# Optimization experiments

Measured on AMD Instinct MI355X. Metric: run time of the kernel, lower is better.

Reference implementation:

```python
import jax, jax.numpy as jnp
import numpy as np

B, N_CTX, NY, NX = 8, 1024, 128, 128
DIM_Y = 2
DOMAIN = 10.0


def setup_inputs() -> dict:
    key = jax.random.key(0)
    k1, k2 = jax.random.split(key)
    X_c = jax.random.uniform(k1, (B, N_CTX, 2), dtype=jnp.float32) * DOMAIN
    Y_c = jax.random.normal(k2, (B, N_CTX, DIM_Y), dtype=jnp.float32)
    ys = jnp.linspace(0.0, DOMAIN, NY, dtype=jnp.float32)
    xs = jnp.linspace(0.0, DOMAIN, NX, dtype=jnp.float32)
    gy, gx = jnp.meshgrid(ys, xs, indexing='ij')  # [NY,NX]
    grid = jnp.stack([gx, gy], axis=-1).reshape(-1, 2)  # [NY*NX, 2]
    log_l_scale = jnp.zeros((1,), dtype=jnp.float32)  # log(1.0)
    return {"X_c": X_c, "Y_c": Y_c, "grid": grid, "log_l_scale": log_l_scale}


def reference(X_c, Y_c, grid, log_l_scale):
    # l_scale = exp(clamp(log_l_scale, -5, 5))
    l = jnp.exp(jnp.clip(log_l_scale[0], -5.0, 5.0))
    # Pairwise squared distances grid-to-context: [B, G, N]
    diff = grid[None, :, None, :] - X_c[:, None, :, :]  # [B,G,N,2]
    d2 = jnp.sum(diff * diff, axis=-1)                  # [B,G,N]
    Gram = jnp.exp(-d2 / (2.0 * l * l))                 # RBF kernel
    # Expand Y with leading ones channel (density channel)
    ones = jnp.ones((B, N_CTX, 1), dtype=Y_c.dtype)
    Expand_Y = jnp.concatenate([ones, Y_c], axis=-1)    # [B,N,3]
    FM = jnp.einsum('bgn,bnc->bgc', Gram, Expand_Y)     # [B,G,3]
    density = FM[..., :1]
    feats = FM[..., 1:] / density                       # normalize by density
    FM = jnp.concatenate([density, feats], axis=-1)
    # reshape to image layout [B, C, NY, NX]
    return FM.reshape(B, NY, NX, DIM_Y + 1).transpose(0, 3, 1, 2)
```

## Files before the change

kernel.cpp:

```cpp
#include <hip/hip_runtime.h>


#define NCTX 1024
#define NG   128
#define NB   8
#define CH   64
#define STR  66

template<int NSPLIT>
__global__ __launch_bounds__(256, 2)
void eds_partial(const float* __restrict__ Xc,
                 const float* __restrict__ Yc,
                 const float* __restrict__ gridp,
                 const float* __restrict__ logl,
                 float* __restrict__ part)
{
    constexpr int SC = NCTX / NSPLIT;
    __shared__ float sEx[64 * STR];
    __shared__ float sEy[64 * STR];

    const int tid  = threadIdx.x;
    const int ixl  = tid & 15;
    const int iyl  = tid >> 4;
    const int lane = tid & 63;
    const int wv   = tid >> 6;

    int blk = blockIdx.x;
    const int s    = blk % NSPLIT;  blk /= NSPLIT;
    const int tile = blk & 3;
    const int b    = blk >> 2;
    const int tx0 = (tile & 1) * 64;
    const int ty0 = (tile >> 1) * 64;

    const float ls = fminf(5.0f, fmaxf(-5.0f, logl[0]));
    const float l  = expf(ls);
    const float scale = -0.7213475204444817f / (l * l);

    float d[16], a[16], c[16];
    #pragma unroll
    for (int i = 0; i < 16; ++i) { d[i] = 0.0f; a[i] = 0.0f; c[i] = 0.0f; }

    for (int ch = 0; ch < SC / CH; ++ch) {
        const int cb = s * SC + ch * CH;
        if (ch) __syncthreads();

        {
            const float gxr = gridp[2 * (tx0 + lane)];
            const float gyr = gridp[2 * ((ty0 + lane) * NG) + 1];
            const float* Xp = Xc + ((size_t)b * NCTX + cb + 16 * wv) * 2;
            float xv[16], yv[16];
            #pragma unroll
            for (int t = 0; t < 8; ++t) {
                const float4 p = ((const float4*)Xp)[t];
                xv[2 * t]     = p.x;  yv[2 * t]     = p.y;
                xv[2 * t + 1] = p.z;  yv[2 * t + 1] = p.w;
            }
            float ex[16], ey[16];
            #pragma unroll
            for (int t = 0; t < 16; ++t) {
                const float dx = gxr - xv[t];
                const float dy = gyr - yv[t];
                ex[t] = exp2f(dx * dx * scale);
                ey[t] = exp2f(dy * dy * scale);
            }
            #pragma unroll
            for (int t = 0; t < 4; ++t) {
                *(float4*)&sEx[lane * STR + 16 * wv + 4 * t] =
                    make_float4(ex[4*t], ex[4*t+1], ex[4*t+2], ex[4*t+3]);
                *(float4*)&sEy[lane * STR + 16 * wv + 4 * t] =
                    make_float4(ey[4*t], ey[4*t+1], ey[4*t+2], ey[4*t+3]);
            }
        }
        __syncthreads();

        const float4* yp = (const float4*)(Yc + ((size_t)b * NCTX + cb) * 2);
        const float* exb = &sEx[ixl * STR];
        const float* eyb = &sEy[iyl * STR];

        #pragma unroll 4
        for (int k = 0; k < CH / 2; ++k) {
            float2 ex[4], ey[4];
            #pragma unroll
            for (int i = 0; i < 4; ++i) ex[i] = *(const float2*)&exb[16 * i * STR + 2 * k];
            #pragma unroll
            for (int j = 0; j < 4; ++j) ey[j] = *(const float2*)&eyb[16 * j * STR + 2 * k];
            const float4 y = yp[k];
            #pragma unroll
            for (int i = 0; i < 4; ++i) {
                #pragma unroll
                for (int j = 0; j < 4; ++j) {
                    const int o = i * 4 + j;
                    float w;
                    w = ex[i].x * ey[j].x;
                    d[o] += w; a[o] = fmaf(w, y.x, a[o]); c[o] = fmaf(w, y.y, c[o]);
                    w = ex[i].y * ey[j].y;
                    d[o] += w; a[o] = fmaf(w, y.z, a[o]); c[o] = fmaf(w, y.w, c[o]);
                }
            }
        }
    }

    const size_t G = (size_t)NG * NG;
    float* P = part + ((size_t)(s * NB + b) * 3) * G;
    #pragma unroll
    for (int i = 0; i < 4; ++i) {
        #pragma unroll
        for (int j = 0; j < 4; ++j) {
            const int o = (ty0 + iyl + 16 * j) * NG + (tx0 + ixl + 16 * i);
            P[        o] = d[i * 4 + j];
            P[G     + o] = a[i * 4 + j];
            P[2 * G + o] = c[i * 4 + j];
        }
    }
}

template<int NSPLIT>
__global__ __launch_bounds__(256)
void eds_combine(const float* __restrict__ part, float* __restrict__ out)
{
    const size_t G = (size_t)NG * NG;
    const int t = blockIdx.x * 256 + threadIdx.x;
    const int b = t >> 12;
    const int o4 = t & 4095;
    float4 d = make_float4(0.f, 0.f, 0.f, 0.f);
    float4 a1 = d, a2 = d;
    #pragma unroll
    for (int s = 0; s < NSPLIT; ++s) {
        const float4* P = (const float4*)(part + ((size_t)(s * NB + b) * 3) * G);
        const float4 pd = P[o4];
        const float4 p1 = P[G / 4 + o4];
        const float4 p2 = P[G / 2 + o4];
        d.x += pd.x; d.y += pd.y; d.z += pd.z; d.w += pd.w;
        a1.x += p1.x; a1.y += p1.y; a1.z += p1.z; a1.w += p1.w;
        a2.x += p2.x; a2.y += p2.y; a2.z += p2.z; a2.w += p2.w;
    }
    float4* O = (float4*)(out + (size_t)b * 3 * G);
    O[o4] = d;
    O[G / 4 + o4] = make_float4(a1.x / d.x, a1.y / d.y, a1.z / d.z, a1.w / d.w);
    O[G / 2 + o4] = make_float4(a2.x / d.x, a2.y / d.y, a2.z / d.z, a2.w / d.w);
}

extern "C" void kernel_launch(void* const* d_in, const int* in_sizes, int n_in,
                              void* d_out, int out_size, void* d_ws, size_t ws_size,
                              hipStream_t stream) {
    const float* Xc = (const float*)d_in[0];
    const float* Yc = (const float*)d_in[1];
    const float* gr = (const float*)d_in[2];
    const float* ll = (const float*)d_in[3];
    float* out  = (float*)d_out;
    float* part = (float*)d_ws;

    const size_t need16 = (size_t)16 * NB * 3 * NG * NG * sizeof(float);
    if (ws_size >= need16) {
        eds_partial<16><<<dim3(NB * 4 * 16), dim3(256), 0, stream>>>(Xc, Yc, gr, ll, part);
        eds_combine<16><<<dim3(NB * NG * NG / 4 / 256), dim3(256), 0, stream>>>(part, out);
    } else {
        eds_partial<4><<<dim3(NB * 4 * 4), dim3(256), 0, stream>>>(Xc, Yc, gr, ll, part);
        eds_combine<4><<<dim3(NB * NG * NG / 4 / 256), dim3(256), 0, stream>>>(part, out);
    }
}
```

Baseline: 87.52 us.

## Drop split-K and combine kernel; fuse normalization into single full-context kernel

Removes the context split and the separate combine pass. Each of 32 blocks now loops over all 1024 context points and writes density and normalized features straight to the output. The inner accumulation is rewritten so weights are folded into FMAs with precomputed ey*y products, and the exp table is filled one context point per lane instead of one grid row per lane. This avoids the partial-buffer round trip and the second launch, but it cuts the grid from 512 blocks to 32, leaving most compute units idle.

```diff
diff --git a/kernel.cpp b/kernel.cpp
--- a/kernel.cpp
+++ b/kernel.cpp
@@ -7,15 +7,13 @@
 #define CH   64
 #define STR  66
 
-template<int NSPLIT>
-__global__ __launch_bounds__(256, 2)
-void eds_partial(const float* __restrict__ Xc,
-                 const float* __restrict__ Yc,
-                 const float* __restrict__ gridp,
-                 const float* __restrict__ logl,
-                 float* __restrict__ part)
+__global__ __launch_bounds__(256, 4)
+void eds_full(const float* __restrict__ Xc,
+              const float* __restrict__ Yc,
+              const float* __restrict__ gridp,
+              const float* __restrict__ logl,
+              float* __restrict__ out)
 {
-    constexpr int SC = NCTX / NSPLIT;
     __shared__ float sEx[64 * STR];
     __shared__ float sEy[64 * STR];
 
@@ -25,12 +23,11 @@
     const int lane = tid & 63;
     const int wv   = tid >> 6;
 
-    int blk = blockIdx.x;
-    const int s    = blk % NSPLIT;  blk /= NSPLIT;
+    const int blk  = blockIdx.x;
     const int tile = blk & 3;
     const int b    = blk >> 2;
-    const int tx0 = (tile & 1) * 64;
-    const int ty0 = (tile >> 1) * 64;
+    const int tx0  = (tile & 1) * 64;
+    const int ty0  = (tile >> 1) * 64;
 
     const float ls = fminf(5.0f, fmaxf(-5.0f, logl[0]));
     const float l  = expf(ls);
@@ -40,44 +37,29 @@
     #pragma unroll
     for (int i = 0; i < 16; ++i) { d[i] = 0.0f; a[i] = 0.0f; c[i] = 0.0f; }
 
-    for (int ch = 0; ch < SC / CH; ++ch) {
-        const int cb = s * SC + ch * CH;
-        if (ch) __syncthreads();
+    for (int c0 = 0; c0 < NCTX; c0 += CH) {
+        if (c0) __syncthreads();
 
         {
-            const float gxr = gridp[2 * (tx0 + lane)];
-            const float gyr = gridp[2 * ((ty0 + lane) * NG) + 1];
-            const float* Xp = Xc + ((size_t)b * NCTX + cb + 16 * wv) * 2;
-            float xv[16], yv[16];
+            const float2 X = ((const float2*)(Xc + ((size_t)b * NCTX + c0) * 2))[lane];
             #pragma unroll
-            for (int t = 0; t < 8; ++t) {
-                const float4 p = ((const float4*)Xp)[t];
-                xv[2 * t]     = p.x;  yv[2 * t]     = p.y;
-                xv[2 * t + 1] = p.z;  yv[2 * t + 1] = p.w;
-            }
-            float ex[16], ey[16];
-            #pragma unroll
-            for (int t = 0; t < 16; ++t) {
-                const float dx = gxr - xv[t];
-                const float dy = gyr - yv[t];
-                ex[t] = exp2f(dx * dx * scale);
-                ey[t] = exp2f(dy * dy * scale);
-            }
-            #pragma unroll
-            for (int t = 0; t < 4; ++t) {
-                *(float4*)&sEx[lane * STR + 16 * wv + 4 * t] =
-                    make_float4(ex[4*t], ex[4*t+1], ex[4*t+2], ex[4*t+3]);
-                *(float4*)&sEy[lane * STR + 16 * wv + 4 * t] =
-                    make_float4(ey[4*t], ey[4*t+1], ey[4*t+2], ey[4*t+3]);
+            for (int r = 0; r < 16; ++r) {
+                const int row = wv * 16 + r;
+                const float gxr = gridp[2 * (tx0 + row)];
+                const float gyr = gridp[2 * ((ty0 + row) * NG) + 1];
+                const float dx = gxr - X.x;
+                const float dy = gyr - X.y;
+                sEx[row * STR + lane] = exp2f(dx * dx * scale);
+                sEy[row * STR + lane] = exp2f(dy * dy * scale);
             }
         }
         __syncthreads();
 
-        const float4* yp = (const float4*)(Yc + ((size_t)b * NCTX + cb) * 2);
+        const float4* yp = (const float4*)(Yc + ((size_t)b * NCTX + c0) * 2);
         const float* exb = &sEx[ixl * STR];
         const float* eyb = &sEy[iyl * STR];
 
-        #pragma unroll 4
+        #pragma unroll 2
         for (int k = 0; k < CH / 2; ++k) {
             float2 ex[4], ey[4];
             #pragma unroll
@@ -85,59 +67,42 @@
             #pragma unroll
             for (int j = 0; j < 4; ++j) ey[j] = *(const float2*)&eyb[16 * j * STR + 2 * k];
             const float4 y = yp[k];
+
+            float e1a[4], e2a[4], e1b[4], e2b[4];
+            #pragma unroll
+            for (int j = 0; j < 4; ++j) {
+                e1a[j] = ey[j].x * y.x;  e2a[j] = ey[j].x * y.y;
+                e1b[j] = ey[j].y * y.z;  e2b[j] = ey[j].y * y.w;
+            }
             #pragma unroll
             for (int i = 0; i < 4; ++i) {
                 #pragma unroll
                 for (int j = 0; j < 4; ++j) {
                     const int o = i * 4 + j;
-                    float w;
-                    w = ex[i].x * ey[j].x;
-                    d[o] += w; a[o] = fmaf(w, y.x, a[o]); c[o] = fmaf(w, y.y, c[o]);
-                    w = ex[i].y * ey[j].y;
-                    d[o] += w; a[o] = fmaf(w, y.z, a[o]); c[o] = fmaf(w, y.w, c[o]);
+                    d[o] = fmaf(ex[i].x, ey[j].x, d[o]);
+                    a[o] = fmaf(ex[i].x, e1a[j], a[o]);
+                    c[o] = fmaf(ex[i].x, e2a[j], c[o]);
+                    d[o] = fmaf(ex[i].y, ey[j].y, d[o]);
+                    a[o] = fmaf(ex[i].y, e1b[j], a[o]);
+                    c[o] = fmaf(ex[i].y, e2b[j], c[o]);
                 }
             }
         }
     }
 
     const size_t G = (size_t)NG * NG;
-    float* P = part + ((size_t)(s * NB + b) * 3) * G;
+    float* O = out + (size_t)b * 3 * G;
     #pragma unroll
     for (int i = 0; i < 4; ++i) {
         #pragma unroll
         for (int j = 0; j < 4; ++j) {
             const int o = (ty0 + iyl + 16 * j) * NG + (tx0 + ixl + 16 * i);
-            P[        o] = d[i * 4 + j];
-            P[G     + o] = a[i * 4 + j];
-            P[2 * G + o] = c[i * 4 + j];
+            const int t = i * 4 + j;
+            O[        o] = d[t];
+            O[G     + o] = a[t] / d[t];
+            O[2 * G + o] = c[t] / d[t];
         }
     }
-}
-
-template<int NSPLIT>
-__global__ __launch_bounds__(256)
-void eds_combine(const float* __restrict__ part, float* __restrict__ out)
-{
-    const size_t G = (size_t)NG * NG;
-    const int t = blockIdx.x * 256 + threadIdx.x;
-    const int b = t >> 12;
-    const int o4 = t & 4095;
-    float4 d = make_float4(0.f, 0.f, 0.f, 0.f);
-    float4 a1 = d, a2 = d;
-    #pragma unroll
-    for (int s = 0; s < NSPLIT; ++s) {
-        const float4* P = (const float4*)(part + ((size_t)(s * NB + b) * 3) * G);
-        const float4 pd = P[o4];
-        const float4 p1 = P[G / 4 + o4];
-        const float4 p2 = P[G / 2 + o4];
-        d.x += pd.x; d.y += pd.y; d.z += pd.z; d.w += pd.w;
-        a1.x += p1.x; a1.y += p1.y; a1.z += p1.z; a1.w += p1.w;
-        a2.x += p2.x; a2.y += p2.y; a2.z += p2.z; a2.w += p2.w;
-    }
-    float4* O = (float4*)(out + (size_t)b * 3 * G);
-    O[o4] = d;
-    O[G / 4 + o4] = make_float4(a1.x / d.x, a1.y / d.y, a1.z / d.z, a1.w / d.w);
-    O[G / 2 + o4] = make_float4(a2.x / d.x, a2.y / d.y, a2.z / d.z, a2.w / d.w);
 }
 
 extern "C" void kernel_launch(void* const* d_in, const int* in_sizes, int n_in,
@@ -147,15 +112,7 @@
     const float* Yc = (const float*)d_in[1];
     const float* gr = (const float*)d_in[2];
     const float* ll = (const float*)d_in[3];
-    float* out  = (float*)d_out;
-    float* part = (float*)d_ws;
+    float* out = (float*)d_out;
 
-    const size_t need16 = (size_t)16 * NB * 3 * NG * NG * sizeof(float);
-    if (ws_size >= need16) {
-        eds_partial<16><<<dim3(NB * 4 * 16), dim3(256), 0, stream>>>(Xc, Yc, gr, ll, part);
-        eds_combine<16><<<dim3(NB * NG * NG / 4 / 256), dim3(256), 0, stream>>>(part, out);
-    } else {
-        eds_partial<4><<<dim3(NB * 4 * 4), dim3(256), 0, stream>>>(Xc, Yc, gr, ll, part);
-        eds_combine<4><<<dim3(NB * NG * NG / 4 / 256), dim3(256), 0, stream>>>(part, out);
-    }
+    eds_full<<<dim3(NB * 4), dim3(256), 0, stream>>>(Xc, Yc, gr, ll, out);
 }
```

Result: slower. 205.9 us (+135.3%).
